# Kernel tuning notes

Measured on AMD Instinct MI355X. Metric: run time of the kernel, lower is better.

## Reference

```python
import jax, jax.numpy as jnp
import numpy as np

B = 131072
SD, AD, HID = 24, 8, 32
NH = SD + AD            # n_heads = 32
UNITS = HID * NH        # 1024


def _xavier(k, shape):
    fan_in, fan_out = shape[-2], shape[-1]
    lim = float(np.sqrt(6.0 / (fan_in + fan_out)))
    return jax.random.uniform(k, shape, jnp.float32, -lim, lim)


def setup_inputs() -> dict:
    key = jax.random.key(0)
    ks = jax.random.split(key, 8)
    return dict(
        state=jax.random.normal(ks[0], (B, SD), jnp.float32),
        action=jax.random.normal(ks[1], (B, AD), jnp.float32),
        # ripple layer 1: per-head Linear(NH -> HID), gate logits init 0 (init_prob=0.5)
        W1=_xavier(ks[2], (NH, NH, HID)), b1=jnp.zeros((NH, HID), jnp.float32), g1=jnp.zeros((NH,), jnp.float32),
        # ripple layer 2: per-head Linear(UNITS -> HID)
        W2=_xavier(ks[3], (NH, UNITS, HID)), b2=jnp.zeros((NH, HID), jnp.float32), g2=jnp.zeros((NH,), jnp.float32),
        # q_network
        Wq1=_xavier(ks[4], (UNITS, 256)), bq1=jnp.zeros((256,), jnp.float32),
        ln1_g=jnp.ones((256,), jnp.float32), ln1_b=jnp.zeros((256,), jnp.float32),
        Wq2=_xavier(ks[5], (256, 128)), bq2=jnp.zeros((128,), jnp.float32),
        ln2_g=jnp.ones((128,), jnp.float32), ln2_b=jnp.zeros((128,), jnp.float32),
        Wq3=_xavier(ks[6], (128, 1)), bq3=jnp.zeros((1,), jnp.float32),
    )


def _ripple(x, W, b, g):
    # x: [B, D]; W: [H, D, K]; per-head linear + tanh, scaled by per-head sigmoid gate
    h = jnp.tanh(jnp.einsum('bd,hdk->bhk', x, W) + b[None])  # [B, H, K]
    h = h * jax.nn.sigmoid(g)[None, :, None]
    return h.reshape(x.shape[0], -1)  # [B, H*K]


def _ln(x, g, b, eps=1e-5):
    mu = jnp.mean(x, -1, keepdims=True)
    var = jnp.mean((x - mu) ** 2, -1, keepdims=True)
    return (x - mu) * jax.lax.rsqrt(var + eps) * g + b


def reference(state, action, W1, b1, g1, W2, b2, g2,
              Wq1, bq1, ln1_g, ln1_b, Wq2, bq2, ln2_g, ln2_b, Wq3, bq3):
    sa = jnp.concatenate([state, action], axis=1)          # [B, SD+AD]
    x = _ripple(sa, W1, b1, g1)                            # [B, UNITS]
    x = _ripple(x, W2, b2, g2)                             # [B, UNITS]
    h = jax.nn.relu(_ln(x @ Wq1 + bq1, ln1_g, ln1_b))      # [B, 256] (dropout = eval identity)
    h = jax.nn.relu(_ln(h @ Wq2 + bq2, ln2_g, ln2_b))      # [B, 128]
    return h @ Wq3 + bq3                                   # [B, 1]
```

## Files before the change

kernel.cpp:

```cpp
#include <hip/hip_runtime.h>
#include <hip/hip_bf16.h>

typedef _Float16 f16x8 __attribute__((ext_vector_type(8)));
typedef _Float16 f16x4 __attribute__((ext_vector_type(4)));
typedef float f32x4 __attribute__((ext_vector_type(4)));

__device__ __forceinline__ float tanh_fast(float x) {
  float e = __expf(2.0f * x);
  return 1.0f - 2.0f * __builtin_amdgcn_rcpf(e + 1.0f);
}
__device__ __forceinline__ float sigmoid_fast(float x) {
  return __builtin_amdgcn_rcpf(1.0f + __expf(-x));
}

__global__ __launch_bounds__(256) void prep_weights(
    const float* __restrict__ W1, const float* __restrict__ W2,
    const float* __restrict__ Wq1, const float* __restrict__ Wq2,
    _Float16* __restrict__ V1p, _Float16* __restrict__ V2p,
    _Float16* __restrict__ T1p, _Float16* __restrict__ T2p) {
  __shared__ float S[32 * 33];
  int b = blockIdx.x, t = threadIdx.x;
  if (b < 2624) {
    const float* in; _Float16* out; int N, nc0, tile, use_pi;
    if (b < 2048) {
      int h = b >> 6, rem = b & 63, ntl = rem >> 5, kt = rem & 31;
      in = W2 + (size_t)h * 32768 + (size_t)kt * 32 * 32;
      N = 32; nc0 = ntl * 16;
      out = V2p; tile = kt * 64 + (h * 2 + ntl); use_pi = 1;
    } else if (b < 2560) {
      int i = b - 2048, nt = i >> 5, kt = i & 31;
      in = Wq1 + (size_t)kt * 32 * 256; N = 256; nc0 = nt * 16;
      out = T1p; tile = kt * 16 + nt; use_pi = 1;
    } else {
      int i = b - 2560, nt = i >> 3, kt = i & 7;
      in = Wq2 + (size_t)kt * 32 * 128; N = 128; nc0 = nt * 16;
      out = T2p; tile = nt * 8 + kt; use_pi = 0;
    }
    if (t < 128) {
      int r = t >> 2, c4 = (t & 3) * 4;
      const float4 v = *(const float4*)(in + (size_t)r * N + nc0 + c4);
      S[r * 17 + c4 + 0] = v.x; S[r * 17 + c4 + 1] = v.y;
      S[r * 17 + c4 + 2] = v.z; S[r * 17 + c4 + 3] = v.w;
    }
    __syncthreads();
    if (t < 128) {
      int w2 = t >> 6, l = t & 63, q = l >> 4, l15 = l & 15;
      f16x4 o;
#pragma unroll
      for (int jj = 0; jj < 4; ++jj) {
        int kl = use_pi ? (q * 4 + jj + w2 * 16) : (q * 8 + w2 * 4 + jj);
        o[jj] = (_Float16)S[kl * 17 + l15];
      }
      *(f16x4*)(out + (size_t)tile * 512 + l * 8 + w2 * 4) = o;
    }
  } else {
    int h = b - 2624;
    const float* in = W1 + h * 1024;
    int cc = t & 31, rr8 = t >> 5;
#pragma unroll
    for (int p = 0; p < 4; ++p) {
      int r = rr8 + p * 8;
      S[cc * 33 + r] = in[r * 32 + cc];
    }
    __syncthreads();
    if (t < 128) {
      int ntl = t >> 6, l = t & 63, q = l >> 4, l15 = l & 15;
      f16x8 o;
#pragma unroll
      for (int j = 0; j < 8; ++j)
        o[j] = (_Float16)S[(ntl * 16 + l15) * 33 + q * 8 + j];
      *(f16x8*)(V1p + (size_t)(h * 2 + ntl) * 512 + l * 8) = o;
    }
  }
}

__global__ __launch_bounds__(512, 2) void k12_fused(
    const float* __restrict__ state, const float* __restrict__ action,
    const _Float16* __restrict__ v1p, const float* __restrict__ b1,
    const float* __restrict__ g1,
    const _Float16* __restrict__ v2p, const float* __restrict__ b2,
    const float* __restrict__ g2,
    _Float16* __restrict__ x2p, int gro, int NRT) {
  __shared__ __align__(16) _Float16 SA[64 * 40];
  __shared__ __align__(16) _Float16 XB[2][8 * 4 * 512];
  int bm = blockIdx.x;
  int t = threadIdx.x, w = t >> 6, l = t & 63, q = l >> 4, l15 = l & 15;
  int m0 = bm * 64;

  {
    int r = t >> 3, qq = t & 7;
    size_t grow = (size_t)(gro + m0 + r);
    const float* src = (qq < 6) ? (state + grow * 24 + qq * 4)
                                : (action + grow * 8 + (qq - 6) * 4);
    float4 v = *(const float4*)src;
    f16x4 h;
    h[0] = (_Float16)v.x; h[1] = (_Float16)v.y;
    h[2] = (_Float16)v.z; h[3] = (_Float16)v.w;
    *(f16x4*)&SA[r * 40 + qq * 4] = h;
  }
  __syncthreads();

  f16x8 asa[4];
#pragma unroll
  for (int p = 0; p < 4; ++p)
    asa[p] = *(const f16x8*)&SA[(p * 16 + l15) * 40 + q * 8];

  const int nt0 = w * 8;
  const _Float16* bBase = v2p + (size_t)nt0 * 512 + (size_t)l * 8;
  f32x4 acc[4][8] = {};

  auto produce = [&](int h, int buf) {
    f16x8 rb0 = *(const f16x8*)(v1p + (size_t)(2 * h) * 512 + l * 8);
    f16x8 rb1 = *(const f16x8*)(v1p + (size_t)(2 * h + 1) * 512 + l * 8);
    float sg = sigmoid_fast(g1[h]);
    f32x4 bs0 = *(const f32x4*)(b1 + h * 32 + q * 4);
    f32x4 bs1 = *(const f32x4*)(b1 + h * 32 + 16 + q * 4);
    _Float16* bw = &XB[buf][(size_t)((h & 7) * 4) * 512 + l * 8];
#pragma unroll
    for (int pp = 0; pp < 4; ++pp) {
      f32x4 d0 = {}, d1 = {};
      d0 = __builtin_amdgcn_mfma_f32_16x16x32_f16(rb0, asa[pp], d0, 0, 0, 0);
      d1 = __builtin_amdgcn_mfma_f32_16x16x32_f16(rb1, asa[pp], d1, 0, 0, 0);
      f16x8 o;
#pragma unroll
      for (int r = 0; r < 4; ++r) {
        o[r]     = (_Float16)(tanh_fast(d0[r] + bs0[r]) * sg);
        o[4 + r] = (_Float16)(tanh_fast(d1[r] + bs1[r]) * sg);
      }
      *(f16x8*)(bw + (size_t)pp * 512) = o;
    }
  };

  f16x8 bb0[4], bb1v[4];
#pragma unroll
  for (int n2 = 0; n2 < 4; ++n2)
    bb0[n2] = *(const f16x8*)(bBase + (size_t)n2 * 512);
#pragma unroll
  for (int n2 = 0; n2 < 4; ++n2)
    bb1v[n2] = *(const f16x8*)(bBase + (size_t)(4 + n2) * 512);
  produce(w, 0);
  __syncthreads();

  f16x8 xab[2][4];
#pragma unroll
  for (int p = 0; p < 4; ++p) {
    const _Float16* buf = XB[p & 1];
#pragma unroll
    for (int mi = 0; mi < 4; ++mi)
      xab[0][mi] = *(const f16x8*)(buf + (size_t)mi * 512 + l * 8);
#pragma unroll
    for (int ktl = 0; ktl < 8; ++ktl) {
      int kt = p * 8 + ktl;
      if (ktl == w && p < 3) produce((p + 1) * 8 + w, (p & 1) ^ 1);
      if (ktl < 7) {
#pragma unroll
        for (int mi = 0; mi < 4; ++mi)
          xab[(ktl + 1) & 1][mi] =
              *(const f16x8*)(buf + (size_t)((ktl + 1) * 4 + mi) * 512 + l * 8);
      }
      __builtin_amdgcn_s_setprio(1);
#pragma unroll
      for (int mi = 0; mi < 4; ++mi)
#pragma unroll
        for (int n2 = 0; n2 < 4; ++n2)
          acc[mi][n2] = __builtin_amdgcn_mfma_f32_16x16x32_f16(
              bb0[n2], xab[ktl & 1][mi], acc[mi][n2], 0, 0, 0);
      if (kt < 31) {
#pragma unroll
        for (int n2 = 0; n2 < 4; ++n2)
          bb0[n2] = *(const f16x8*)(bBase + (size_t)((kt + 1) * 64 + n2) * 512);
      }
#pragma unroll
      for (int mi = 0; mi < 4; ++mi)
#pragma unroll
        for (int n2 = 0; n2 < 4; ++n2)
          acc[mi][4 + n2] = __builtin_amdgcn_mfma_f32_16x16x32_f16(
              bb1v[n2], xab[ktl & 1][mi], acc[mi][4 + n2], 0, 0, 0);
      if (kt < 31) {
#pragma unroll
        for (int n2 = 0; n2 < 4; ++n2)
          bb1v[n2] = *(const f16x8*)(bBase + (size_t)((kt + 1) * 64 + 4 + n2) * 512);
      }
      __builtin_amdgcn_s_setprio(0);
    }
    if (p < 3) __syncthreads();
  }

#pragma unroll
  for (int mi = 0; mi < 4; ++mi) {
    int rt = bm * 4 + mi;
#pragma unroll
    for (int p2 = 0; p2 < 4; ++p2) {
      int kc2 = (nt0 >> 1) + p2;
      float sg2 = sigmoid_fast(g2[kc2]);
      f32x4 c0 = *(const f32x4*)(b2 + kc2 * 32 + q * 4);
      f32x4 c1 = *(const f32x4*)(b2 + kc2 * 32 + 16 + q * 4);
      f16x8 o;
#pragma unroll
      for (int r = 0; r < 4; ++r) {
        o[r]     = (_Float16)(tanh_fast(acc[mi][2 * p2][r] + c0[r]) * sg2);
        o[4 + r] = (_Float16)(tanh_fast(acc[mi][2 * p2 + 1][r] + c1[r]) * sg2);
      }
      *(f16x8*)(x2p + ((size_t)kc2 * NRT + rt) * 512 + l * 8) = o;
    }
  }
}

__global__ __launch_bounds__(512, 3) void k3_head(
    const _Float16* __restrict__ x2p, const _Float16* __restrict__ t1p,
    const _Float16* __restrict__ t2p,
    const float* __restrict__ bq1, const float* __restrict__ ln1g, const float* __restrict__ ln1b,
    const float* __restrict__ bq2, const float* __restrict__ ln2g, const float* __restrict__ ln2b,
    const float* __restrict__ wq3, const float* __restrict__ bq3,
    float* __restrict__ out, int NRT, int SROWS) {
  __shared__ __align__(16) _Float16 y1h[128 * 264];
  __shared__ float redA[128 * 4], redB[128 * 4];
  __shared__ float meanv[128], rstdv[128];
  int bm = blockIdx.x;
  int t = threadIdx.x, w = t >> 6, l = t & 63, q = l >> 4, l15 = l & 15;
  int wr = w >> 2, wc = w & 3;

  int gt = bm * 8;
  int slice = 0;
  if (gt >= NRT) { slice = 1; gt -= NRT; }
  int rt0 = gt + wr * 4;

  f32x4 acc[4][4] = {};
  const size_t aStep = (size_t)NRT * 512;
  const _Float16* aP = x2p + (size_t)slice * SROWS * 1024 + (size_t)rt0 * 512 + (size_t)l * 8;
  const _Float16* bP = t1p + (size_t)(wc * 4) * 512 + (size_t)l * 8;

  f16x8 a0[4], a1[4], b0[4], b1[4];
#pragma unroll
  for (int mi = 0; mi < 4; ++mi) a0[mi] = *(const f16x8*)(aP + mi * 512);
#pragma unroll
  for (int ni = 0; ni < 4; ++ni) b0[ni] = *(const f16x8*)(bP + ni * 512);
#pragma unroll
  for (int mi = 0; mi < 4; ++mi) a1[mi] = *(const f16x8*)(aP + aStep + mi * 512);
#pragma unroll
  for (int ni = 0; ni < 4; ++ni) b1[ni] = *(const f16x8*)(bP + 8192 + ni * 512);
  aP += 2 * aStep; bP += 16384;

  for (int kt = 0; kt < 32; kt += 2) {
#pragma unroll
    for (int mi = 0; mi < 4; ++mi)
#pragma unroll
      for (int ni = 0; ni < 4; ++ni)
        acc[mi][ni] = __builtin_amdgcn_mfma_f32_16x16x32_f16(a0[mi], b0[ni], acc[mi][ni], 0, 0, 0);
    if (kt < 30) {
#pragma unroll
      for (int mi = 0; mi < 4; ++mi) a0[mi] = *(const f16x8*)(aP + mi * 512);
#pragma unroll
      for (int ni = 0; ni < 4; ++ni) b0[ni] = *(const f16x8*)(bP + ni * 512);
    }
#pragma unroll
    for (int mi = 0; mi < 4; ++mi)
#pragma unroll
      for (int ni = 0; ni < 4; ++ni)
        acc[mi][ni] = __builtin_amdgcn_mfma_f32_16x16x32_f16(a1[mi], b1[ni], acc[mi][ni], 0, 0, 0);
    if (kt < 30) {
#pragma unroll
      for (int mi = 0; mi < 4; ++mi) a1[mi] = *(const f16x8*)(aP + aStep + mi * 512);
#pragma unroll
      for (int ni = 0; ni < 4; ++ni) b1[ni] = *(const f16x8*)(bP + 8192 + ni * 512);
      aP += 2 * aStep; bP += 16384;
    }
  }

#pragma unroll
  for (int ni = 0; ni < 4; ++ni) {
    int col = wc * 64 + ni * 16 + l15;
    float b = bq1[col];
#pragma unroll
    for (int mi = 0; mi < 4; ++mi)
#pragma unroll
      for (int r = 0; r < 4; ++r) acc[mi][ni][r] += b;
  }
#pragma unroll
  for (int mi = 0; mi < 4; ++mi)
#pragma unroll
    for (int r = 0; r < 4; ++r) {
      int row = wr * 64 + mi * 16 + q * 4 + r;
      float s = 0.f, sq = 0.f;
#pragma unroll
      for (int ni = 0; ni < 4; ++ni) { float v = acc[mi][ni][r]; s += v; sq += v * v; }
#pragma unroll
      for (int off = 1; off < 16; off <<= 1) { s += __shfl_xor(s, off); sq += __shfl_xor(sq, off); }
      if (l15 == 0) { redA[row * 4 + wc] = s; redB[row * 4 + wc] = sq; }
    }
  __syncthreads();
  if (t < 128) {
    float s  = redA[t * 4] + redA[t * 4 + 1] + redA[t * 4 + 2] + redA[t * 4 + 3];
    float sq = redB[t * 4] + redB[t * 4 + 1] + redB[t * 4 + 2] + redB[t * 4 + 3];
    float mean = s * (1.0f / 256.0f);
    float var = sq * (1.0f / 256.0f) - mean * mean;
    meanv[t] = mean; rstdv[t] = rsqrtf(var + 1e-5f);
  }
  __syncthreads();
#pragma unroll
  for (int mi = 0; mi < 4; ++mi)
#pragma unroll
    for (int ni = 0; ni < 4; ++ni)
#pragma unroll
      for (int r = 0; r < 4; ++r) {
        int row = wr * 64 + mi * 16 + q * 4 + r;
        int col = wc * 64 + ni * 16 + l15;
        float y = (acc[mi][ni][r] - meanv[row]) * rstdv[row] * ln1g[col] + ln1b[col];
        y = fmaxf(y, 0.f);
        y1h[row * 264 + col] = (_Float16)y;
      }
  __syncthreads();

  f32x4 a2[4][2] = {};
  for (int kt = 0; kt < 8; ++kt) {
    f16x8 af2[4];
#pragma unroll
    for (int mi = 0; mi < 4; ++mi)
      af2[mi] = *(const f16x8*)&y1h[(wr * 64 + mi * 16 + l15) * 264 + kt * 32 + q * 8];
#pragma unroll
    for (int ni = 0; ni < 2; ++ni) {
      f16x8 bf = *(const f16x8*)(t2p + (size_t)(wc * 2 + ni) * 4096 + kt * 512 + l * 8);
#pragma unroll
      for (int mi = 0; mi < 4; ++mi)
        a2[mi][ni] = __builtin_amdgcn_mfma_f32_16x16x32_f16(af2[mi], bf, a2[mi][ni], 0, 0, 0);
    }
  }
#pragma unroll
  for (int ni = 0; ni < 2; ++ni) {
    int col = wc * 32 + ni * 16 + l15;
    float b = bq2[col];
#pragma unroll
    for (int mi = 0; mi < 4; ++mi)
#pragma unroll
      for (int r = 0; r < 4; ++r) a2[mi][ni][r] += b;
  }
  __syncthreads();
#pragma unroll
  for (int mi = 0; mi < 4; ++mi)
#pragma unroll
    for (int r = 0; r < 4; ++r) {
      int row = wr * 64 + mi * 16 + q * 4 + r;
      float s = 0.f, sq = 0.f;
#pragma unroll
      for (int ni = 0; ni < 2; ++ni) { float v = a2[mi][ni][r]; s += v; sq += v * v; }
#pragma unroll
      for (int off = 1; off < 16; off <<= 1) { s += __shfl_xor(s, off); sq += __shfl_xor(sq, off); }
      if (l15 == 0) { redA[row * 4 + wc] = s; redB[row * 4 + wc] = sq; }
    }
  __syncthreads();
  if (t < 128) {
    float s  = redA[t * 4] + redA[t * 4 + 1] + redA[t * 4 + 2] + redA[t * 4 + 3];
    float sq = redB[t * 4] + redB[t * 4 + 1] + redB[t * 4 + 2] + redB[t * 4 + 3];
    float mean = s * (1.0f / 128.0f);
    float var = sq * (1.0f / 128.0f) - mean * mean;
    meanv[t] = mean; rstdv[t] = rsqrtf(var + 1e-5f);
  }
  __syncthreads();
#pragma unroll
  for (int mi = 0; mi < 4; ++mi)
#pragma unroll
    for (int r = 0; r < 4; ++r) {
      int row = wr * 64 + mi * 16 + q * 4 + r;
      float pr = 0.f;
#pragma unroll
      for (int ni = 0; ni < 2; ++ni) {
        int col = wc * 32 + ni * 16 + l15;
        float y = (a2[mi][ni][r] - meanv[row]) * rstdv[row] * ln2g[col] + ln2b[col];
        y = fmaxf(y, 0.f);
        pr += y * wq3[col];
      }
#pragma unroll
      for (int off = 1; off < 16; off <<= 1) pr += __shfl_xor(pr, off);
      if (l15 == 0) redA[row * 4 + wc] = pr;
    }
  __syncthreads();
  if (t < 128)
    out[bm * 128 + t] = redA[t * 4] + redA[t * 4 + 1] + redA[t * 4 + 2] + redA[t * 4 + 3] + bq3[0];
}

extern "C" void kernel_launch(void* const* d_in, const int* in_sizes, int n_in,
                              void* d_out, int out_size, void* d_ws, size_t ws_size,
                              hipStream_t stream) {
  const float* state  = (const float*)d_in[0];
  const float* action = (const float*)d_in[1];
  const float* W1  = (const float*)d_in[2];
  const float* b1  = (const float*)d_in[3];
  const float* g1  = (const float*)d_in[4];
  const float* W2  = (const float*)d_in[5];
  const float* b2  = (const float*)d_in[6];
  const float* g2  = (const float*)d_in[7];
  const float* Wq1 = (const float*)d_in[8];
  const float* bq1 = (const float*)d_in[9];
  const float* ln1g = (const float*)d_in[10];
  const float* ln1b = (const float*)d_in[11];
  const float* Wq2 = (const float*)d_in[12];
  const float* bq2 = (const float*)d_in[13];
  const float* ln2g = (const float*)d_in[14];
  const float* ln2b = (const float*)d_in[15];
  const float* Wq3 = (const float*)d_in[16];
  const float* bq3 = (const float*)d_in[17];
  int B = in_sizes[0] / 24;

  char* ws = (char*)d_ws;
  _Float16* V1p = (_Float16*)(ws);
  _Float16* V2p = (_Float16*)(ws + 65536);
  _Float16* T1p = (_Float16*)(ws + 65536 + 2097152);
  _Float16* T2p = (_Float16*)(ws + 65536 + 2097152 + 524288);
  size_t woff = (65536 + 2097152 + 524288 + 65536 + 4095) & ~(size_t)4095;

  size_t avail = ws_size > woff ? ws_size - woff : 0;
  long rows = (long)(avail / 2048);
  if (rows > 32768) rows = 32768;
  rows &= ~127L;
  if (rows < 128) rows = 128;
  int S = (int)rows;
  _Float16* x2 = (_Float16*)(ws + woff);
  int NRT = S / 16;

  prep_weights<<<2656, 256, 0, stream>>>(W1, W2, Wq1, Wq2, V1p, V2p, T1p, T2p);

  for (int r0 = 0; r0 < B; r0 += S) {
    int Sc = S < (B - r0) ? S : (B - r0);
    int nbm = Sc / 128;
    k12_fused<<<dim3(Sc / 64), 512, 0, stream>>>(state, action, V1p, b1, g1,
                                                 V2p, b2, g2, x2, r0, NRT);
    k3_head<<<dim3(nbm), 512, 0, stream>>>(x2, T1p, T2p, bq1, ln1g, ln1b,
                                           bq2, ln2g, ln2b, Wq3, bq3,
                                           (float*)d_out + r0, NRT, S);
  }
}
```

Measured before the change: 575.5 us.

## Fuse ripple layers and Q-head into one kernel via LDS-staged activations

Merges the two-kernel pipeline into a single kernel. Each 64-row block now keeps the second ripple layer's fp16 output in shared memory (reusing the XB buffer, half at a time) and runs the Q-network GEMMs, layer norms and final projection in place. This removes the global-memory round trip of the 1024-wide activation, the chunked launch loop and the workspace sizing logic. In exchange, each block uses more LDS (an extra y1h buffer), which may lower occupancy. The head GEMMs now use a smaller 64-row tile that reloads Wq1 per block, with extra barriers between the half-staged passes.

```diff
diff --git a/kernel.cpp b/kernel.cpp
--- a/kernel.cpp
+++ b/kernel.cpp
@@ -74,22 +74,33 @@
   }
 }
 
-__global__ __launch_bounds__(512, 2) void k12_fused(
+__global__ __launch_bounds__(512, 2) void k12q(
     const float* __restrict__ state, const float* __restrict__ action,
     const _Float16* __restrict__ v1p, const float* __restrict__ b1,
     const float* __restrict__ g1,
     const _Float16* __restrict__ v2p, const float* __restrict__ b2,
     const float* __restrict__ g2,
-    _Float16* __restrict__ x2p, int gro, int NRT) {
+    const _Float16* __restrict__ t1p, const _Float16* __restrict__ t2p,
+    const float* __restrict__ bq1, const float* __restrict__ ln1g,
+    const float* __restrict__ ln1b,
+    const float* __restrict__ bq2, const float* __restrict__ ln2g,
+    const float* __restrict__ ln2b,
+    const float* __restrict__ wq3, const float* __restrict__ bq3,
+    float* __restrict__ out) {
   __shared__ __align__(16) _Float16 SA[64 * 40];
   __shared__ __align__(16) _Float16 XB[2][8 * 4 * 512];
+  __shared__ __align__(16) _Float16 y1h[64 * 264];
+  __shared__ float redA[64 * 8], redB[64 * 8];
+  __shared__ float meanv[64], rstdv[64];
+  _Float16* x2h = &XB[0][0];
+
   int bm = blockIdx.x;
   int t = threadIdx.x, w = t >> 6, l = t & 63, q = l >> 4, l15 = l & 15;
   int m0 = bm * 64;
 
   {
     int r = t >> 3, qq = t & 7;
-    size_t grow = (size_t)(gro + m0 + r);
+    size_t grow = (size_t)(m0 + r);
     const float* src = (qq < 6) ? (state + grow * 24 + qq * 4)
                                 : (action + grow * 8 + (qq - 6) * 4);
     float4 v = *(const float4*)src;
@@ -186,112 +197,104 @@
     if (p < 3) __syncthreads();
   }
 
-#pragma unroll
-  for (int mi = 0; mi < 4; ++mi) {
-    int rt = bm * 4 + mi;
-#pragma unroll
-    for (int p2 = 0; p2 < 4; ++p2) {
-      int kc2 = (nt0 >> 1) + p2;
-      float sg2 = sigmoid_fast(g2[kc2]);
-      f32x4 c0 = *(const f32x4*)(b2 + kc2 * 32 + q * 4);
-      f32x4 c1 = *(const f32x4*)(b2 + kc2 * 32 + 16 + q * 4);
-      f16x8 o;
-#pragma unroll
-      for (int r = 0; r < 4; ++r) {
-        o[r]     = (_Float16)(tanh_fast(acc[mi][2 * p2][r] + c0[r]) * sg2);
-        o[4 + r] = (_Float16)(tanh_fast(acc[mi][2 * p2 + 1][r] + c1[r]) * sg2);
-      }
-      *(f16x8*)(x2p + ((size_t)kc2 * NRT + rt) * 512 + l * 8) = o;
-    }
-  }
-}
-
-__global__ __launch_bounds__(512, 3) void k3_head(
-    const _Float16* __restrict__ x2p, const _Float16* __restrict__ t1p,
-    const _Float16* __restrict__ t2p,
-    const float* __restrict__ bq1, const float* __restrict__ ln1g, const float* __restrict__ ln1b,
-    const float* __restrict__ bq2, const float* __restrict__ ln2g, const float* __restrict__ ln2b,
-    const float* __restrict__ wq3, const float* __restrict__ bq3,
-    float* __restrict__ out, int NRT, int SROWS) {
-  __shared__ __align__(16) _Float16 y1h[128 * 264];
-  __shared__ float redA[128 * 4], redB[128 * 4];
-  __shared__ float meanv[128], rstdv[128];
-  int bm = blockIdx.x;
-  int t = threadIdx.x, w = t >> 6, l = t & 63, q = l >> 4, l15 = l & 15;
-  int wr = w >> 2, wc = w & 3;
-
-  int gt = bm * 8;
-  int slice = 0;
-  if (gt >= NRT) { slice = 1; gt -= NRT; }
-  int rt0 = gt + wr * 4;
-
-  f32x4 acc[4][4] = {};
-  const size_t aStep = (size_t)NRT * 512;
-  const _Float16* aP = x2p + (size_t)slice * SROWS * 1024 + (size_t)rt0 * 512 + (size_t)l * 8;
-  const _Float16* bP = t1p + (size_t)(wc * 4) * 512 + (size_t)l * 8;
-
-  f16x8 a0[4], a1[4], b0[4], b1[4];
-#pragma unroll
-  for (int mi = 0; mi < 4; ++mi) a0[mi] = *(const f16x8*)(aP + mi * 512);
-#pragma unroll
-  for (int ni = 0; ni < 4; ++ni) b0[ni] = *(const f16x8*)(bP + ni * 512);
-#pragma unroll
-  for (int mi = 0; mi < 4; ++mi) a1[mi] = *(const f16x8*)(aP + aStep + mi * 512);
-#pragma unroll
-  for (int ni = 0; ni < 4; ++ni) b1[ni] = *(const f16x8*)(bP + 8192 + ni * 512);
-  aP += 2 * aStep; bP += 16384;
-
-  for (int kt = 0; kt < 32; kt += 2) {
-#pragma unroll
-    for (int mi = 0; mi < 4; ++mi)
-#pragma unroll
-      for (int ni = 0; ni < 4; ++ni)
-        acc[mi][ni] = __builtin_amdgcn_mfma_f32_16x16x32_f16(a0[mi], b0[ni], acc[mi][ni], 0, 0, 0);
-    if (kt < 30) {
-#pragma unroll
-      for (int mi = 0; mi < 4; ++mi) a0[mi] = *(const f16x8*)(aP + mi * 512);
-#pragma unroll
-      for (int ni = 0; ni < 4; ++ni) b0[ni] = *(const f16x8*)(bP + ni * 512);
-    }
-#pragma unroll
-    for (int mi = 0; mi < 4; ++mi)
-#pragma unroll
-      for (int ni = 0; ni < 4; ++ni)
-        acc[mi][ni] = __builtin_amdgcn_mfma_f32_16x16x32_f16(a1[mi], b1[ni], acc[mi][ni], 0, 0, 0);
-    if (kt < 30) {
-#pragma unroll
-      for (int mi = 0; mi < 4; ++mi) a1[mi] = *(const f16x8*)(aP + aStep + mi * 512);
-#pragma unroll
-      for (int ni = 0; ni < 4; ++ni) b1[ni] = *(const f16x8*)(bP + 8192 + ni * 512);
-      aP += 2 * aStep; bP += 16384;
-    }
-  }
-
-#pragma unroll
-  for (int ni = 0; ni < 4; ++ni) {
-    int col = wc * 64 + ni * 16 + l15;
+  __syncthreads();
+
+  if (w < 4) {
+#pragma unroll
+    for (int mi = 0; mi < 4; ++mi)
+#pragma unroll
+      for (int p2 = 0; p2 < 4; ++p2) {
+        int kc2 = w * 4 + p2;
+        float sg2 = sigmoid_fast(g2[kc2]);
+        f32x4 c0 = *(const f32x4*)(b2 + kc2 * 32 + q * 4);
+        f32x4 c1 = *(const f32x4*)(b2 + kc2 * 32 + 16 + q * 4);
+        f16x8 o;
+#pragma unroll
+        for (int r = 0; r < 4; ++r) {
+          o[r]     = (_Float16)(tanh_fast(acc[mi][2 * p2][r] + c0[r]) * sg2);
+          o[4 + r] = (_Float16)(tanh_fast(acc[mi][2 * p2 + 1][r] + c1[r]) * sg2);
+        }
+        *(f16x8*)(x2h + (size_t)(kc2 * 4 + mi) * 512 + l * 8) = o;
+      }
+  }
+  __syncthreads();
+
+  f32x4 acc2[4][2] = {};
+  for (int kt = 0; kt < 16; ++kt) {
+    f16x8 a[4];
+#pragma unroll
+    for (int mi = 0; mi < 4; ++mi)
+      a[mi] = *(const f16x8*)(x2h + (size_t)(kt * 4 + mi) * 512 + l * 8);
+    f16x8 bf0 = *(const f16x8*)(t1p + (size_t)(kt * 16 + w * 2) * 512 + l * 8);
+    f16x8 bf1 = *(const f16x8*)(t1p + (size_t)(kt * 16 + w * 2 + 1) * 512 + l * 8);
+#pragma unroll
+    for (int mi = 0; mi < 4; ++mi) {
+      acc2[mi][0] = __builtin_amdgcn_mfma_f32_16x16x32_f16(a[mi], bf0, acc2[mi][0], 0, 0, 0);
+      acc2[mi][1] = __builtin_amdgcn_mfma_f32_16x16x32_f16(a[mi], bf1, acc2[mi][1], 0, 0, 0);
+    }
+  }
+  __syncthreads();
+
+  if (w >= 4) {
+#pragma unroll
+    for (int mi = 0; mi < 4; ++mi)
+#pragma unroll
+      for (int p2 = 0; p2 < 4; ++p2) {
+        int kc2 = w * 4 + p2;
+        float sg2 = sigmoid_fast(g2[kc2]);
+        f32x4 c0 = *(const f32x4*)(b2 + kc2 * 32 + q * 4);
+        f32x4 c1 = *(const f32x4*)(b2 + kc2 * 32 + 16 + q * 4);
+        f16x8 o;
+#pragma unroll
+        for (int r = 0; r < 4; ++r) {
+          o[r]     = (_Float16)(tanh_fast(acc[mi][2 * p2][r] + c0[r]) * sg2);
+          o[4 + r] = (_Float16)(tanh_fast(acc[mi][2 * p2 + 1][r] + c1[r]) * sg2);
+        }
+        *(f16x8*)(x2h + (size_t)((kc2 - 16) * 4 + mi) * 512 + l * 8) = o;
+      }
+  }
+  __syncthreads();
+
+  for (int kt = 16; kt < 32; ++kt) {
+    f16x8 a[4];
+#pragma unroll
+    for (int mi = 0; mi < 4; ++mi)
+      a[mi] = *(const f16x8*)(x2h + (size_t)((kt - 16) * 4 + mi) * 512 + l * 8);
+    f16x8 bf0 = *(const f16x8*)(t1p + (size_t)(kt * 16 + w * 2) * 512 + l * 8);
+    f16x8 bf1 = *(const f16x8*)(t1p + (size_t)(kt * 16 + w * 2 + 1) * 512 + l * 8);
+#pragma unroll
+    for (int mi = 0; mi < 4; ++mi) {
+      acc2[mi][0] = __builtin_amdgcn_mfma_f32_16x16x32_f16(a[mi], bf0, acc2[mi][0], 0, 0, 0);
+      acc2[mi][1] = __builtin_amdgcn_mfma_f32_16x16x32_f16(a[mi], bf1, acc2[mi][1], 0, 0, 0);
+    }
+  }
+
+#pragma unroll
+  for (int ni = 0; ni < 2; ++ni) {
+    int col = w * 32 + ni * 16 + l15;
     float b = bq1[col];
 #pragma unroll
     for (int mi = 0; mi < 4; ++mi)
 #pragma unroll
-      for (int r = 0; r < 4; ++r) acc[mi][ni][r] += b;
+      for (int r = 0; r < 4; ++r) acc2[mi][ni][r] += b;
   }
 #pragma unroll
   for (int mi = 0; mi < 4; ++mi)
 #pragma unroll
     for (int r = 0; r < 4; ++r) {
-      int row = wr * 64 + mi * 16 + q * 4 + r;
+      int row = mi * 16 + q * 4 + r;
       float s = 0.f, sq = 0.f;
 #pragma unroll
-      for (int ni = 0; ni < 4; ++ni) { float v = acc[mi][ni][r]; s += v; sq += v * v; }
+      for (int ni = 0; ni < 2; ++ni) { float v = acc2[mi][ni][r]; s += v; sq += v * v; }
 #pragma unroll
       for (int off = 1; off < 16; off <<= 1) { s += __shfl_xor(s, off); sq += __shfl_xor(sq, off); }
-      if (l15 == 0) { redA[row * 4 + wc] = s; redB[row * 4 + wc] = sq; }
-    }
-  __syncthreads();
-  if (t < 128) {
-    float s  = redA[t * 4] + redA[t * 4 + 1] + redA[t * 4 + 2] + redA[t * 4 + 3];
-    float sq = redB[t * 4] + redB[t * 4 + 1] + redB[t * 4 + 2] + redB[t * 4 + 3];
+      if (l15 == 0) { redA[row * 8 + w] = s; redB[row * 8 + w] = sq; }
+    }
+  __syncthreads();
+  if (t < 64) {
+    float s = 0.f, sq = 0.f;
+#pragma unroll
+    for (int i = 0; i < 8; ++i) { s += redA[t * 8 + i]; sq += redB[t * 8 + i]; }
     float mean = s * (1.0f / 256.0f);
     float var = sq * (1.0f / 256.0f) - mean * mean;
     meanv[t] = mean; rstdv[t] = rsqrtf(var + 1e-5f);
@@ -300,57 +303,52 @@
 #pragma unroll
   for (int mi = 0; mi < 4; ++mi)
 #pragma unroll
-    for (int ni = 0; ni < 4; ++ni)
+    for (int ni = 0; ni < 2; ++ni)
 #pragma unroll
       for (int r = 0; r < 4; ++r) {
-        int row = wr * 64 + mi * 16 + q * 4 + r;
-        int col = wc * 64 + ni * 16 + l15;
-        float y = (acc[mi][ni][r] - meanv[row]) * rstdv[row] * ln1g[col] + ln1b[col];
+        int row = mi * 16 + q * 4 + r;
+        int col = w * 32 + ni * 16 + l15;
+        float y = (acc2[mi][ni][r] - meanv[row]) * rstdv[row] * ln1g[col] + ln1b[col];
         y = fmaxf(y, 0.f);
         y1h[row * 264 + col] = (_Float16)y;
       }
   __syncthreads();
 
-  f32x4 a2[4][2] = {};
+  f32x4 a3[4] = {};
   for (int kt = 0; kt < 8; ++kt) {
-    f16x8 af2[4];
-#pragma unroll
-    for (int mi = 0; mi < 4; ++mi)
-      af2[mi] = *(const f16x8*)&y1h[(wr * 64 + mi * 16 + l15) * 264 + kt * 32 + q * 8];
-#pragma unroll
-    for (int ni = 0; ni < 2; ++ni) {
-      f16x8 bf = *(const f16x8*)(t2p + (size_t)(wc * 2 + ni) * 4096 + kt * 512 + l * 8);
-#pragma unroll
-      for (int mi = 0; mi < 4; ++mi)
-        a2[mi][ni] = __builtin_amdgcn_mfma_f32_16x16x32_f16(af2[mi], bf, a2[mi][ni], 0, 0, 0);
-    }
-  }
-#pragma unroll
-  for (int ni = 0; ni < 2; ++ni) {
-    int col = wc * 32 + ni * 16 + l15;
+    f16x8 af[4];
+#pragma unroll
+    for (int mi = 0; mi < 4; ++mi)
+      af[mi] = *(const f16x8*)&y1h[(mi * 16 + l15) * 264 + kt * 32 + q * 8];
+    f16x8 bf = *(const f16x8*)(t2p + (size_t)(w * 8 + kt) * 512 + l * 8);
+#pragma unroll
+    for (int mi = 0; mi < 4; ++mi)
+      a3[mi] = __builtin_amdgcn_mfma_f32_16x16x32_f16(af[mi], bf, a3[mi], 0, 0, 0);
+  }
+  {
+    int col = w * 16 + l15;
     float b = bq2[col];
 #pragma unroll
     for (int mi = 0; mi < 4; ++mi)
 #pragma unroll
-      for (int r = 0; r < 4; ++r) a2[mi][ni][r] += b;
+      for (int r = 0; r < 4; ++r) a3[mi][r] += b;
   }
   __syncthreads();
 #pragma unroll
   for (int mi = 0; mi < 4; ++mi)
 #pragma unroll
     for (int r = 0; r < 4; ++r) {
-      int row = wr * 64 + mi * 16 + q * 4 + r;
-      float s = 0.f, sq = 0.f;
-#pragma unroll
-      for (int ni = 0; ni < 2; ++ni) { float v = a2[mi][ni][r]; s += v; sq += v * v; }
+      int row = mi * 16 + q * 4 + r;
+      float s = a3[mi][r], sq = s * s;
 #pragma unroll
       for (int off = 1; off < 16; off <<= 1) { s += __shfl_xor(s, off); sq += __shfl_xor(sq, off); }
-      if (l15 == 0) { redA[row * 4 + wc] = s; redB[row * 4 + wc] = sq; }
-    }
-  __syncthreads();
-  if (t < 128) {
-    float s  = redA[t * 4] + redA[t * 4 + 1] + redA[t * 4 + 2] + redA[t * 4 + 3];
-    float sq = redB[t * 4] + redB[t * 4 + 1] + redB[t * 4 + 2] + redB[t * 4 + 3];
+      if (l15 == 0) { redA[row * 8 + w] = s; redB[row * 8 + w] = sq; }
+    }
+  __syncthreads();
+  if (t < 64) {
+    float s = 0.f, sq = 0.f;
+#pragma unroll
+    for (int i = 0; i < 8; ++i) { s += redA[t * 8 + i]; sq += redB[t * 8 + i]; }
     float mean = s * (1.0f / 128.0f);
     float var = sq * (1.0f / 128.0f) - mean * mean;
     meanv[t] = mean; rstdv[t] = rsqrtf(var + 1e-5f);
@@ -360,22 +358,22 @@
   for (int mi = 0; mi < 4; ++mi)
 #pragma unroll
     for (int r = 0; r < 4; ++r) {
-      int row = wr * 64 + mi * 16 + q * 4 + r;
-      float pr = 0.f;
-#pragma unroll
-      for (int ni = 0; ni < 2; ++ni) {
-        int col = wc * 32 + ni * 16 + l15;
-        float y = (a2[mi][ni][r] - meanv[row]) * rstdv[row] * ln2g[col] + ln2b[col];
-        y = fmaxf(y, 0.f);
-        pr += y * wq3[col];
-      }
+      int row = mi * 16 + q * 4 + r;
+      int col = w * 16 + l15;
+      float y = (a3[mi][r] - meanv[row]) * rstdv[row] * ln2g[col] + ln2b[col];
+      y = fmaxf(y, 0.f);
+      float pr = y * wq3[col];
 #pragma unroll
       for (int off = 1; off < 16; off <<= 1) pr += __shfl_xor(pr, off);
-      if (l15 == 0) redA[row * 4 + wc] = pr;
-    }
-  __syncthreads();
-  if (t < 128)
-    out[bm * 128 + t] = redA[t * 4] + redA[t * 4 + 1] + redA[t * 4 + 2] + redA[t * 4 + 3] + bq3[0];
+      if (l15 == 0) redA[row * 8 + w] = pr;
+    }
+  __syncthreads();
+  if (t < 64) {
+    float s = 0.f;
+#pragma unroll
+    for (int i = 0; i < 8; ++i) s += redA[t * 8 + i];
+    out[m0 + t] = s + bq3[0];
+  }
 }
 
 extern "C" void kernel_launch(void* const* d_in, const int* in_sizes, int n_in,
@@ -406,26 +404,12 @@
   _Float16* V2p = (_Float16*)(ws + 65536);
   _Float16* T1p = (_Float16*)(ws + 65536 + 2097152);
   _Float16* T2p = (_Float16*)(ws + 65536 + 2097152 + 524288);
-  size_t woff = (65536 + 2097152 + 524288 + 65536 + 4095) & ~(size_t)4095;
-
-  size_t avail = ws_size > woff ? ws_size - woff : 0;
-  long rows = (long)(avail / 2048);
-  if (rows > 32768) rows = 32768;
-  rows &= ~127L;
-  if (rows < 128) rows = 128;
-  int S = (int)rows;
-  _Float16* x2 = (_Float16*)(ws + woff);
-  int NRT = S / 16;
 
   prep_weights<<<2656, 256, 0, stream>>>(W1, W2, Wq1, Wq2, V1p, V2p, T1p, T2p);
 
-  for (int r0 = 0; r0 < B; r0 += S) {
-    int Sc = S < (B - r0) ? S : (B - r0);
-    int nbm = Sc / 128;
-    k12_fused<<<dim3(Sc / 64), 512, 0, stream>>>(state, action, V1p, b1, g1,
-                                                 V2p, b2, g2, x2, r0, NRT);
-    k3_head<<<dim3(nbm), 512, 0, stream>>>(x2, T1p, T2p, bq1, ln1g, ln1b,
-                                           bq2, ln2g, ln2b, Wq3, bq3,
-                                           (float*)d_out + r0, NRT, S);
-  }
+  int nb = B / 64;
+  k12q<<<dim3(nb), 512, 0, stream>>>(state, action, V1p, b1, g1,
+                                     V2p, b2, g2, T1p, T2p,
+                                     bq1, ln1g, ln1b, bq2, ln2g, ln2b,
+                                     Wq3, bq3, (float*)d_out);
 }
```

Measured after the change: 935.6 us. 1.63x slower.
